# Kernel tuning notes

Hardware: AMD Instinct MI355X
Metric: run time of the kernel (lower is better)

## Reference

```python
import jax, jax.numpy as jnp
import numpy as np

PI = np.pi


def _apply_1q(state, gate, wire, n):
    # state: [B, 2**n] complex64; gate: [2,2] (shared) or [B,2,2] (per-sample)
    # PennyLane convention: wire 0 is the most-significant bit of the state index.
    B = state.shape[0]
    left, right = 2 ** wire, 2 ** (n - wire - 1)
    s = state.reshape(B, left, 2, right)
    if gate.ndim == 2:
        s = jnp.einsum('kl,balr->bakr', gate, s)
    else:
        s = jnp.einsum('bkl,balr->bakr', gate, s)
    return s.reshape(B, -1)


def _apply_cz(state, wire, n):
    # CZ on (wire, wire+1): flip sign of |..11..> amplitudes
    B = state.shape[0]
    left, right = 2 ** wire, 2 ** (n - wire - 2)
    s = state.reshape(B, left, 2, 2, right)
    s = s.at[:, :, 1, 1, :].multiply(-1.0)
    return s.reshape(B, -1)


def _ry_batched(theta):
    # theta: [B] -> [B,2,2] complex RY(theta)
    h = 0.5 * theta
    c, s = jnp.cos(h), jnp.sin(h)
    g = jnp.stack([jnp.stack([c, -s], -1), jnp.stack([s, c], -1)], -2)
    return g.astype(jnp.complex64)


def _rot(phi, theta, omega):
    # Rot = RZ(omega) @ RY(theta) @ RZ(phi)
    c, s = jnp.cos(0.5 * theta), jnp.sin(0.5 * theta)
    e_mm = jnp.exp(-0.5j * (phi + omega))
    e_pm = jnp.exp(0.5j * (phi - omega))
    e_mp = jnp.exp(-0.5j * (phi - omega))
    e_pp = jnp.exp(0.5j * (phi + omega))
    g = jnp.stack([jnp.stack([e_mm * c, -e_pm * s]), jnp.stack([e_mp * s, e_pp * c])])
    return g.astype(jnp.complex64)


def _simulate(enc, weights):
    # enc: [B, n_qubits] in [-1,1]; weights: [n_layers, n_qubits, 3]
    n_layers, n, _ = weights.shape
    B = enc.shape[0]
    state = jnp.zeros((B, 2 ** n), jnp.complex64).at[:, 0].set(1.0)
    ry = [_ry_batched(enc[:, i] * PI) for i in range(n)]
    for l in range(n_layers):
        for i in range(n):
            state = _apply_1q(state, ry[i], i, n)
        for i in range(n):
            state = _apply_1q(state, _rot(weights[l, i, 0], weights[l, i, 1], weights[l, i, 2]), i, n)
        for i in range(n - 1):
            state = _apply_cz(state, i, n)
    for i in range(n):
        state = _apply_1q(state, ry[i], i, n)
    probs = state.real ** 2 + state.imag ** 2  # [B, 2**n]
    # <Z_i> = sum_k probs[k] * (-1)^bit_i(k), wire 0 = MSB
    bits = (jnp.arange(2 ** n)[None, :] >> (n - 1 - jnp.arange(n))[:, None]) & 1
    signs = (1 - 2 * bits).astype(probs.dtype)  # [n, 2**n]
    return probs @ signs.T  # [B, n]


def setup_inputs() -> dict:
    B, D, NQ, NL, NA = 32768, 16, 8, 4, 4
    key = jax.random.key(0)
    ks = jax.random.split(key, 6)

    def lin(k, o, i):
        b = 1.0 / np.sqrt(i)
        k1, k2 = jax.random.split(k)
        return (jax.random.uniform(k1, (o, i), jnp.float32, -b, b),
                jax.random.uniform(k2, (o,), jnp.float32, -b, b))

    enc_w1, enc_b1 = lin(ks[1], 8, D)
    enc_w2, enc_b2 = lin(ks[2], NQ, 8)
    dec_w1, dec_b1 = lin(ks[3], 8, NQ)
    dec_w2, dec_b2 = lin(ks[4], NA, 8)
    q_weights = jax.random.uniform(ks[5], (NL, NQ, 3), jnp.float32, 0.0, 2.0 * PI)
    x = jax.random.normal(ks[0], (B, D), jnp.float32)
    return {"x": x, "enc_w1": enc_w1, "enc_b1": enc_b1, "enc_w2": enc_w2, "enc_b2": enc_b2,
            "q_weights": q_weights, "dec_w1": dec_w1, "dec_b1": dec_b1, "dec_w2": dec_w2, "dec_b2": dec_b2}


def reference(x, enc_w1, enc_b1, enc_w2, enc_b2, q_weights, dec_w1, dec_b1, dec_w2, dec_b2):
    h = jax.nn.relu(x @ enc_w1.T + enc_b1)
    enc = jnp.tanh(h @ enc_w2.T + enc_b2)          # [B, n_qubits]
    q = _simulate(enc, q_weights)                  # [B, n_qubits] PauliZ expvals
    h2 = jax.nn.relu(q @ dec_w1.T + dec_b1)
    return h2 @ dec_w2.T + dec_b2                  # [B, n_actions]
```

## Files before the change

kernel.cpp:

```cpp
#include <hip/hip_runtime.h>
#include <math.h>


#define PI_F 3.14159265358979323846f

typedef float v2f __attribute__((ext_vector_type(2)));

struct C2 { float re, im; };
__device__ __forceinline__ C2 cmul(C2 a, C2 b) {
    C2 r;
    r.re = fmaf(a.re, b.re, -a.im * b.im);
    r.im = fmaf(a.re, b.im,  a.im * b.re);
    return r;
}

__device__ __forceinline__ v2f pk_mul(v2f a, v2f b) {
    v2f d; asm("v_pk_mul_f32 %0, %1, %2" : "=v"(d) : "v"(a), "v"(b)); return d;
}
__device__ __forceinline__ v2f pk_mul_neg(v2f a, v2f b) {
    v2f d; asm("v_pk_mul_f32 %0, %1, %2 neg_lo:[1,0] neg_hi:[1,0]"
               : "=v"(d) : "v"(a), "v"(b)); return d;
}
__device__ __forceinline__ v2f pk_fma(v2f a, v2f b, v2f c) {
    v2f d; asm("v_pk_fma_f32 %0, %1, %2, %3" : "=v"(d) : "v"(a), "v"(b), "v"(c)); return d;
}
__device__ __forceinline__ v2f pk_fma_nn(v2f a, v2f b, v2f c) {
    v2f d; asm("v_pk_fma_f32 %0, %1, %2, %3 neg_lo:[1,0,0] neg_hi:[1,0,0]"
               : "=v"(d) : "v"(a), "v"(b), "v"(c)); return d;
}
__device__ __forceinline__ v2f pk_fma_swl(v2f a, v2f b, v2f c) {
    v2f d; asm("v_pk_fma_f32 %0, %1, %2, %3 op_sel:[0,1,0] op_sel_hi:[1,0,1] neg_lo:[1,0,0]"
               : "=v"(d) : "v"(a), "v"(b), "v"(c)); return d;
}
__device__ __forceinline__ v2f pk_fma_swh(v2f a, v2f b, v2f c) {
    v2f d; asm("v_pk_fma_f32 %0, %1, %2, %3 op_sel:[0,1,0] op_sel_hi:[1,0,1] neg_hi:[1,0,0]"
               : "=v"(d) : "v"(a), "v"(b), "v"(c)); return d;
}

template<int CTRL>
__device__ __forceinline__ float dppf(float x) {
    int xi = __float_as_int(x);
    int r = __builtin_amdgcn_update_dpp(xi, xi, CTRL, 0xF, 0xF, false);
    return __int_as_float(r);
}
template<int M>
__device__ __forceinline__ float lxor(float x) {
    if constexpr (M == 1)      return dppf<0xB1>(x);
    else if constexpr (M == 2) return dppf<0x4E>(x);
    else if constexpr (M == 4) return __int_as_float(
        __builtin_amdgcn_ds_swizzle(__float_as_int(x), 0x101F));
    else                       return dppf<0x128>(x);
}

__device__ __forceinline__ void build_G(const float* __restrict__ c_lds, int g,
                                        float cc, float ss,
                                        v2f& arr, v2f& aii, v2f& brr, v2f& bii) {
    const float4 c0 = *(const float4*)(c_lds + 4 * g);
    float ar = fmaf(c0.x, cc, -c0.z * ss);
    float ai = fmaf(c0.y, cc,  c0.w * ss);
    float br = fmaf(c0.z, cc,  c0.x * ss);
    float bi = fmaf(c0.w, cc, -c0.y * ss);
    arr = (v2f){ar, ar}; aii = (v2f){ai, ai};
    brr = (v2f){br, br}; bii = (v2f){bi, bi};
}

template<int ST>
__device__ __forceinline__ void su2_inlane(v2f arr, v2f aii, v2f brr, v2f bii,
                                           v2f z[16]) {
#pragma unroll
    for (int t = 0; t < 16; t++) {
        if ((t & ST) == 0) {
            const int u = t + ST;
            v2f x = z[t], y = z[u];
            v2f nx = pk_mul(arr, x);
            nx = pk_fma_swl(aii, x, nx);
            nx = pk_fma_nn (brr, y, nx);
            nx = pk_fma_swl(bii, y, nx);
            v2f ny = pk_mul(brr, x);
            ny = pk_fma_swl(bii, x, ny);
            ny = pk_fma   (arr, y, ny);
            ny = pk_fma_swh(aii, y, ny);
            z[t] = nx; z[u] = ny;
        }
    }
}

template<int ST>
__device__ __forceinline__ void ry_inlane(v2f cc, v2f ss, v2f z[16]) {
#pragma unroll
    for (int t = 0; t < 16; t++) {
        if ((t & ST) == 0) {
            const int u = t + ST;
            v2f x = z[t], y = z[u];
            z[t] = pk_fma_nn(ss, y, pk_mul(cc, x));
            z[u] = pk_fma   (cc, y, pk_mul(ss, x));
        }
    }
}

__device__ __constant__ const bool CZNEG[16] =
    { false,false,false,true,  false,false,true,false,
      false,false,false,true,  true, true, false,true };

__global__ __launch_bounds__(128) void qdqn_kernel(
    const float* __restrict__ x,
    const float* __restrict__ ew1, const float* __restrict__ eb1,
    const float* __restrict__ ew2, const float* __restrict__ eb2,
    const float* __restrict__ qw,
    const float* __restrict__ dw1, const float* __restrict__ db1,
    const float* __restrict__ dw2, const float* __restrict__ db2,
    float* __restrict__ out, int B, int NL) {
    __shared__ __align__(16) float c_lds[32 * 4];
    __shared__ __align__(16) v2f tbuf[2 * 4 * 288];

    const int tid = threadIdx.x;
    const int n_gates = NL * 8;

    if (tid < n_gates) {
        const int g = tid;
        float phi = qw[3 * g + 0], th = qw[3 * g + 1], om = qw[3 * g + 2];
        float c = __cosf(0.5f * th), s = __sinf(0.5f * th);
        float A = 0.5f * (phi + om), Bb = 0.5f * (phi - om);
        float* o = c_lds + 4 * g;
        o[0] =  __cosf(A) * c;  o[1] = -__sinf(A) * c;
        o[2] =  __cosf(Bb) * s; o[3] = -__sinf(Bb) * s;
    }
    __syncthreads();

    const int wave = tid >> 6;
    const int lane = tid & 63;
    const int grp = lane >> 4;
    const int L = lane & 15;
    int s = blockIdx.x * 8 + wave * 4 + grp;
    if (s >= B) s = B - 1;
    v2f* tb = &tbuf[(wave * 4 + grp) * 288];

    float xv[16];
    const float4* xp = (const float4*)(x + s * 16);
#pragma unroll
    for (int i = 0; i < 4; i++) {
        float4 v = xp[i];
        xv[4*i] = v.x; xv[4*i+1] = v.y; xv[4*i+2] = v.z; xv[4*i+3] = v.w;
    }
    float hbuf[8];
#pragma unroll
    for (int j = 0; j < 8; j++) {
        float a = eb1[j];
#pragma unroll
        for (int i = 0; i < 16; i++) a = fmaf(ew1[j * 16 + i], xv[i], a);
        hbuf[j] = fmaxf(a, 0.0f);
    }
    float cq[8], sq[8];
#pragma unroll
    for (int q = 0; q < 8; q++) {
        float a = eb2[q];
#pragma unroll
        for (int j = 0; j < 8; j++) a = fmaf(ew2[q * 8 + j], hbuf[j], a);
        float e = 1.0f - __fdividef(2.0f, __expf(2.0f * a) + 1.0f);
        float ang = e * (0.5f * PI_F);
        cq[q] = __cosf(ang);
        sq[q] = __sinf(ang);
    }

    const int L0 = L & 1, L1b = (L >> 1) & 1, L2b = (L >> 2) & 1, L3b = (L >> 3) & 1;
    const int cnt = (L3b & L2b) + (L2b & L1b) + (L1b & L0);
    const float mL = (cnt & 1) ? -1.0f : 1.0f;
    const float mH = L0 ? -mL : mL;
    const float mO = L3b ? -mL : mL;
    const v2f mL2 = (v2f){mL, mL}, mH2 = (v2f){mH, mH}, mO2 = (v2f){mO, mO};

    v2f z[16];
    {
        C2 P; P.re = 1.0f; P.im = 0.0f;
        C2 F[4][2];
#pragma unroll
        for (int q = 0; q < 8; q++) {
            const float4 c0 = *(const float4*)(c_lds + 4 * q);
            float ar = fmaf(c0.x, cq[q], -c0.z * sq[q]);
            float ai = fmaf(c0.y, cq[q],  c0.w * sq[q]);
            float br = fmaf(c0.z, cq[q],  c0.x * sq[q]);
            float bi = fmaf(c0.w, cq[q], -c0.y * sq[q]);
            if (q < 4) {
                const bool hi = (L >> (3 - q)) & 1;
                C2 f; f.re = hi ? br : ar; f.im = hi ? bi : ai;
                P = cmul(P, f);
            } else {
                F[q-4][0].re = ar; F[q-4][0].im = ai;
                F[q-4][1].re = br; F[q-4][1].im = bi;
            }
        }
        C2 A0 = cmul(P, F[0][0]), A1 = cmul(P, F[0][1]);
        C2 Bv[4];
        Bv[0] = cmul(A0, F[1][0]); Bv[1] = cmul(A0, F[1][1]);
        Bv[2] = cmul(A1, F[1][0]); Bv[3] = cmul(A1, F[1][1]);
        C2 Cv[8];
#pragma unroll
        for (int i = 0; i < 8; i++) Cv[i] = cmul(Bv[i >> 1], F[2][i & 1]);
#pragma unroll
        for (int t = 0; t < 16; t++) {
            C2 v = cmul(Cv[t >> 1], F[3][t & 1]);
            float m = (t < 8) ? mL : mH;
            m = CZNEG[t] ? -m : m;
            z[t].x = v.re * m;
            z[t].y = v.im * m;
        }
    }

    auto transpose = [&]() {
        float4* wrow = (float4*)(tb + L * 18);
#pragma unroll
        for (int k = 0; k < 8; k++)
            wrow[k] = make_float4(z[2*k].x, z[2*k].y, z[2*k+1].x, z[2*k+1].y);
        __builtin_amdgcn_wave_barrier();
#pragma unroll
        for (int j = 0; j < 16; j++) z[j] = tb[j * 18 + L];
        __builtin_amdgcn_wave_barrier();
    };

    auto cz_A = [&]() {
#pragma unroll
        for (int t = 0; t < 16; t++) {
            v2f m = (t < 8) ? mL2 : mH2;
            z[t] = CZNEG[t] ? pk_mul_neg(m, z[t]) : pk_mul(m, z[t]);
        }
    };
    auto cz_B = [&]() {
#pragma unroll
        for (int j = 0; j < 16; j++) {
            v2f m = (j & 1) ? mO2 : mL2;
            z[j] = CZNEG[j] ? pk_mul_neg(m, z[j]) : pk_mul(m, z[j]);
        }
    };

    v2f arr, aii, brr, bii;
    bool inB = false;
    for (int l = 1; l < NL; l++) {
        const int g0 = l * 8;
        if (!inB) {
            build_G(c_lds, g0+4, cq[4], sq[4], arr, aii, brr, bii); su2_inlane<8>(arr, aii, brr, bii, z);
            build_G(c_lds, g0+5, cq[5], sq[5], arr, aii, brr, bii); su2_inlane<4>(arr, aii, brr, bii, z);
            build_G(c_lds, g0+6, cq[6], sq[6], arr, aii, brr, bii); su2_inlane<2>(arr, aii, brr, bii, z);
            build_G(c_lds, g0+7, cq[7], sq[7], arr, aii, brr, bii); su2_inlane<1>(arr, aii, brr, bii, z);
            transpose();
            build_G(c_lds, g0+0, cq[0], sq[0], arr, aii, brr, bii); su2_inlane<8>(arr, aii, brr, bii, z);
            build_G(c_lds, g0+1, cq[1], sq[1], arr, aii, brr, bii); su2_inlane<4>(arr, aii, brr, bii, z);
            build_G(c_lds, g0+2, cq[2], sq[2], arr, aii, brr, bii); su2_inlane<2>(arr, aii, brr, bii, z);
            build_G(c_lds, g0+3, cq[3], sq[3], arr, aii, brr, bii); su2_inlane<1>(arr, aii, brr, bii, z);
            cz_B();
            inB = true;
        } else {
            build_G(c_lds, g0+0, cq[0], sq[0], arr, aii, brr, bii); su2_inlane<8>(arr, aii, brr, bii, z);
            build_G(c_lds, g0+1, cq[1], sq[1], arr, aii, brr, bii); su2_inlane<4>(arr, aii, brr, bii, z);
            build_G(c_lds, g0+2, cq[2], sq[2], arr, aii, brr, bii); su2_inlane<2>(arr, aii, brr, bii, z);
            build_G(c_lds, g0+3, cq[3], sq[3], arr, aii, brr, bii); su2_inlane<1>(arr, aii, brr, bii, z);
            transpose();
            build_G(c_lds, g0+4, cq[4], sq[4], arr, aii, brr, bii); su2_inlane<8>(arr, aii, brr, bii, z);
            build_G(c_lds, g0+5, cq[5], sq[5], arr, aii, brr, bii); su2_inlane<4>(arr, aii, brr, bii, z);
            build_G(c_lds, g0+6, cq[6], sq[6], arr, aii, brr, bii); su2_inlane<2>(arr, aii, brr, bii, z);
            build_G(c_lds, g0+7, cq[7], sq[7], arr, aii, brr, bii); su2_inlane<1>(arr, aii, brr, bii, z);
            cz_A();
            inB = false;
        }
    }

    {
        v2f cc, ss;
        if (inB) {
            cc=(v2f){cq[0],cq[0]}; ss=(v2f){sq[0],sq[0]}; ry_inlane<8>(cc, ss, z);
            cc=(v2f){cq[1],cq[1]}; ss=(v2f){sq[1],sq[1]}; ry_inlane<4>(cc, ss, z);
            cc=(v2f){cq[2],cq[2]}; ss=(v2f){sq[2],sq[2]}; ry_inlane<2>(cc, ss, z);
            cc=(v2f){cq[3],cq[3]}; ss=(v2f){sq[3],sq[3]}; ry_inlane<1>(cc, ss, z);
            transpose();
            cc=(v2f){cq[4],cq[4]}; ss=(v2f){sq[4],sq[4]}; ry_inlane<8>(cc, ss, z);
            cc=(v2f){cq[5],cq[5]}; ss=(v2f){sq[5],sq[5]}; ry_inlane<4>(cc, ss, z);
            cc=(v2f){cq[6],cq[6]}; ss=(v2f){sq[6],sq[6]}; ry_inlane<2>(cc, ss, z);
            cc=(v2f){cq[7],cq[7]}; ss=(v2f){sq[7],sq[7]}; ry_inlane<1>(cc, ss, z);
        } else {
            cc=(v2f){cq[4],cq[4]}; ss=(v2f){sq[4],sq[4]}; ry_inlane<8>(cc, ss, z);
            cc=(v2f){cq[5],cq[5]}; ss=(v2f){sq[5],sq[5]}; ry_inlane<4>(cc, ss, z);
            cc=(v2f){cq[6],cq[6]}; ss=(v2f){sq[6],sq[6]}; ry_inlane<2>(cc, ss, z);
            cc=(v2f){cq[7],cq[7]}; ss=(v2f){sq[7],sq[7]}; ry_inlane<1>(cc, ss, z);
            transpose();
            cc=(v2f){cq[0],cq[0]}; ss=(v2f){sq[0],sq[0]}; ry_inlane<8>(cc, ss, z);
            cc=(v2f){cq[1],cq[1]}; ss=(v2f){sq[1],sq[1]}; ry_inlane<4>(cc, ss, z);
            cc=(v2f){cq[2],cq[2]}; ss=(v2f){sq[2],sq[2]}; ry_inlane<2>(cc, ss, z);
            cc=(v2f){cq[3],cq[3]}; ss=(v2f){sq[3],sq[3]}; ry_inlane<1>(cc, ss, z);
            transpose();
        }
    }

    float p[16];
#pragma unroll
    for (int t = 0; t < 16; t++) p[t] = fmaf(z[t].x, z[t].x, z[t].y * z[t].y);

    float e0 = p[0]+p[1],  e1 = p[2]+p[3],  e2 = p[4]+p[5],  e3 = p[6]+p[7];
    float e4 = p[8]+p[9],  e5 = p[10]+p[11], e6 = p[12]+p[13], e7 = p[14]+p[15];
    float q0 = e0+e1, q1 = e2+e3, q2 = e4+e5, q3 = e6+e7;
    float h0 = q0+q1, h1 = q2+q3;
    float sumP = h0 + h1;

    float zv[8];
#pragma unroll
    for (int w = 0; w < 4; w++)
        zv[w] = ((L >> (3 - w)) & 1) ? -sumP : sumP;
    zv[4] = h0 - h1;
    zv[5] = (q0 - q1) + (q2 - q3);
    zv[6] = (e0 - e1) + (e2 - e3) + (e4 - e5) + (e6 - e7);
    zv[7] = (p[0]-p[1]) + (p[2]-p[3]) + (p[4]-p[5]) + (p[6]-p[7])
          + (p[8]-p[9]) + (p[10]-p[11]) + (p[12]-p[13]) + (p[14]-p[15]);

#pragma unroll
    for (int w = 0; w < 8; w++) zv[w] += lxor<1>(zv[w]);
#pragma unroll
    for (int w = 0; w < 8; w++) zv[w] += lxor<2>(zv[w]);
#pragma unroll
    for (int w = 0; w < 8; w++) zv[w] += lxor<4>(zv[w]);
#pragma unroll
    for (int w = 0; w < 8; w++) zv[w] += lxor<8>(zv[w]);

    float h2[8];
#pragma unroll
    for (int j = 0; j < 8; j++) {
        float a = db1[j];
#pragma unroll
        for (int w = 0; w < 8; w++) a = fmaf(dw1[j * 8 + w], zv[w], a);
        h2[j] = fmaxf(a, 0.0f);
    }
    if (L < 4) {
        float a = db2[L];
#pragma unroll
        for (int j = 0; j < 8; j++) a = fmaf(dw2[L * 8 + j], h2[j], a);
        out[s * 4 + L] = a;
    }
}

extern "C" void kernel_launch(void* const* d_in, const int* in_sizes, int n_in,
                              void* d_out, int out_size, void* d_ws, size_t ws_size,
                              hipStream_t stream) {
    const float* x   = (const float*)d_in[0];
    const float* ew1 = (const float*)d_in[1];
    const float* eb1 = (const float*)d_in[2];
    const float* ew2 = (const float*)d_in[3];
    const float* eb2 = (const float*)d_in[4];
    const float* qw  = (const float*)d_in[5];
    const float* dw1 = (const float*)d_in[6];
    const float* db1 = (const float*)d_in[7];
    const float* dw2 = (const float*)d_in[8];
    const float* db2 = (const float*)d_in[9];
    float* out = (float*)d_out;

    int B = in_sizes[0] / 16;
    int n_gates = in_sizes[5] / 3;
    int NL = n_gates / 8;

    int blocks = (B + 7) / 8;
    qdqn_kernel<<<blocks, 128, 0, stream>>>(x, ew1, eb1, ew2, eb2, qw,
                                            dw1, db1, dw2, db2, out, B, NL);
}
```

Baseline: 121.6 us.

## Replace LDS transposes with cross-lane DPP/swizzle gate application on high qubits

The LDS-based transpose, which moved the state between two layouts, is removed. The four high qubits are now applied directly across lanes using DPP/ds_swizzle xor exchanges, with sign masks folded into the gate coefficients. This drops the shared-memory staging buffer and the layout-parity tracking, and the block size grows from 128 to 256 threads with 16 samples per block. In exchange, every element of each high-qubit gate now needs cross-lane moves plus more packed FMAs than the in-lane butterfly.

```diff
diff --git a/kernel.cpp b/kernel.cpp
--- a/kernel.cpp
+++ b/kernel.cpp
@@ -12,6 +12,9 @@
     r.re = fmaf(a.re, b.re, -a.im * b.im);
     r.im = fmaf(a.re, b.im,  a.im * b.re);
     return r;
+}
+__device__ __forceinline__ float fxor(float x, int m) {
+    return __int_as_float(__float_as_int(x) ^ m);
 }
 
 __device__ __forceinline__ v2f pk_mul(v2f a, v2f b) {
@@ -52,16 +55,30 @@
     else                       return dppf<0x128>(x);
 }
 
-__device__ __forceinline__ void build_G(const float* __restrict__ c_lds, int g,
+__device__ __forceinline__ void load_G2(const float* __restrict__ c_lds, int g,
                                         float cc, float ss,
-                                        v2f& arr, v2f& aii, v2f& brr, v2f& bii) {
+                                        float& ar, float& ai, float& br, float& bi) {
     const float4 c0 = *(const float4*)(c_lds + 4 * g);
-    float ar = fmaf(c0.x, cc, -c0.z * ss);
-    float ai = fmaf(c0.y, cc,  c0.w * ss);
-    float br = fmaf(c0.z, cc,  c0.x * ss);
-    float bi = fmaf(c0.w, cc, -c0.y * ss);
-    arr = (v2f){ar, ar}; aii = (v2f){ai, ai};
-    brr = (v2f){br, br}; bii = (v2f){bi, bi};
+    ar = fmaf(c0.x, cc, -c0.z * ss);
+    ai = fmaf(c0.y, cc,  c0.w * ss);
+    br = fmaf(c0.z, cc,  c0.x * ss);
+    bi = fmaf(c0.w, cc, -c0.y * ss);
+}
+
+template<int M>
+__device__ __forceinline__ void su2_cross(v2f cSr, v2f cSi, v2f cOr, v2f cOi,
+                                          v2f z[16]) {
+#pragma unroll
+    for (int t = 0; t < 16; t++) {
+        v2f p;
+        p.x = lxor<M>(z[t].x);
+        p.y = lxor<M>(z[t].y);
+        v2f n = pk_mul(cSr, z[t]);
+        n = pk_fma_swl(cSi, z[t], n);
+        n = pk_fma   (cOr, p, n);
+        n = pk_fma_swl(cOi, p, n);
+        z[t] = n;
+    }
 }
 
 template<int ST>
@@ -85,6 +102,16 @@
     }
 }
 
+template<int M>
+__device__ __forceinline__ void ry_cross(v2f cc, v2f cO, v2f z[16]) {
+#pragma unroll
+    for (int t = 0; t < 16; t++) {
+        v2f p;
+        p.x = lxor<M>(z[t].x);
+        p.y = lxor<M>(z[t].y);
+        z[t] = pk_fma(cO, p, pk_mul(cc, z[t]));
+    }
+}
 template<int ST>
 __device__ __forceinline__ void ry_inlane(v2f cc, v2f ss, v2f z[16]) {
 #pragma unroll
@@ -102,7 +129,7 @@
     { false,false,false,true,  false,false,true,false,
       false,false,false,true,  true, true, false,true };
 
-__global__ __launch_bounds__(128) void qdqn_kernel(
+__global__ __launch_bounds__(256) void qdqn_kernel(
     const float* __restrict__ x,
     const float* __restrict__ ew1, const float* __restrict__ eb1,
     const float* __restrict__ ew2, const float* __restrict__ eb2,
@@ -111,7 +138,6 @@
     const float* __restrict__ dw2, const float* __restrict__ db2,
     float* __restrict__ out, int B, int NL) {
     __shared__ __align__(16) float c_lds[32 * 4];
-    __shared__ __align__(16) v2f tbuf[2 * 4 * 288];
 
     const int tid = threadIdx.x;
     const int n_gates = NL * 8;
@@ -127,13 +153,10 @@
     }
     __syncthreads();
 
-    const int wave = tid >> 6;
     const int lane = tid & 63;
-    const int grp = lane >> 4;
     const int L = lane & 15;
-    int s = blockIdx.x * 8 + wave * 4 + grp;
+    int s = blockIdx.x * 16 + (tid >> 4);
     if (s >= B) s = B - 1;
-    v2f* tb = &tbuf[(wave * 4 + grp) * 288];
 
     float xv[16];
     const float4* xp = (const float4*)(x + s * 16);
@@ -162,12 +185,19 @@
         sq[q] = __sinf(ang);
     }
 
+    int hiM[4], loM[4];
+#pragma unroll
+    for (int q = 0; q < 4; q++) {
+        int hi = (L >> (3 - q)) & 1;
+        hiM[q] = hi << 31;
+        loM[q] = hiM[q] ^ 0x80000000;
+    }
+
     const int L0 = L & 1, L1b = (L >> 1) & 1, L2b = (L >> 2) & 1, L3b = (L >> 3) & 1;
     const int cnt = (L3b & L2b) + (L2b & L1b) + (L1b & L0);
     const float mL = (cnt & 1) ? -1.0f : 1.0f;
     const float mH = L0 ? -mL : mL;
-    const float mO = L3b ? -mL : mL;
-    const v2f mL2 = (v2f){mL, mL}, mH2 = (v2f){mH, mH}, mO2 = (v2f){mO, mO};
+    const v2f mL2 = (v2f){mL, mL}, mH2 = (v2f){mH, mH};
 
     v2f z[16];
     {
@@ -175,11 +205,8 @@
         C2 F[4][2];
 #pragma unroll
         for (int q = 0; q < 8; q++) {
-            const float4 c0 = *(const float4*)(c_lds + 4 * q);
-            float ar = fmaf(c0.x, cq[q], -c0.z * sq[q]);
-            float ai = fmaf(c0.y, cq[q],  c0.w * sq[q]);
-            float br = fmaf(c0.z, cq[q],  c0.x * sq[q]);
-            float bi = fmaf(c0.w, cq[q], -c0.y * sq[q]);
+            float ar, ai, br, bi;
+            load_G2(c_lds, q, cq[q], sq[q], ar, ai, br, bi);
             if (q < 4) {
                 const bool hi = (L >> (3 - q)) & 1;
                 C2 f; f.re = hi ? br : ar; f.im = hi ? bi : ai;
@@ -206,87 +233,50 @@
         }
     }
 
-    auto transpose = [&]() {
-        float4* wrow = (float4*)(tb + L * 18);
-#pragma unroll
-        for (int k = 0; k < 8; k++)
-            wrow[k] = make_float4(z[2*k].x, z[2*k].y, z[2*k+1].x, z[2*k+1].y);
-        __builtin_amdgcn_wave_barrier();
-#pragma unroll
-        for (int j = 0; j < 16; j++) z[j] = tb[j * 18 + L];
-        __builtin_amdgcn_wave_barrier();
-    };
-
-    auto cz_A = [&]() {
+    for (int l = 1; l < NL; l++) {
+        const int g0 = l * 8;
+        float ar, ai, br, bi;
+        load_G2(c_lds, g0+0, cq[0], sq[0], ar, ai, br, bi);
+        su2_cross<8>((v2f){ar,ar}, (v2f){fxor(ai,hiM[0]),fxor(ai,hiM[0])},
+                     (v2f){fxor(br,loM[0]),fxor(br,loM[0])}, (v2f){bi,bi}, z);
+        load_G2(c_lds, g0+1, cq[1], sq[1], ar, ai, br, bi);
+        su2_cross<4>((v2f){ar,ar}, (v2f){fxor(ai,hiM[1]),fxor(ai,hiM[1])},
+                     (v2f){fxor(br,loM[1]),fxor(br,loM[1])}, (v2f){bi,bi}, z);
+        load_G2(c_lds, g0+2, cq[2], sq[2], ar, ai, br, bi);
+        su2_cross<2>((v2f){ar,ar}, (v2f){fxor(ai,hiM[2]),fxor(ai,hiM[2])},
+                     (v2f){fxor(br,loM[2]),fxor(br,loM[2])}, (v2f){bi,bi}, z);
+        load_G2(c_lds, g0+3, cq[3], sq[3], ar, ai, br, bi);
+        su2_cross<1>((v2f){ar,ar}, (v2f){fxor(ai,hiM[3]),fxor(ai,hiM[3])},
+                     (v2f){fxor(br,loM[3]),fxor(br,loM[3])}, (v2f){bi,bi}, z);
+        load_G2(c_lds, g0+4, cq[4], sq[4], ar, ai, br, bi);
+        su2_inlane<8>((v2f){ar,ar}, (v2f){ai,ai}, (v2f){br,br}, (v2f){bi,bi}, z);
+        load_G2(c_lds, g0+5, cq[5], sq[5], ar, ai, br, bi);
+        su2_inlane<4>((v2f){ar,ar}, (v2f){ai,ai}, (v2f){br,br}, (v2f){bi,bi}, z);
+        load_G2(c_lds, g0+6, cq[6], sq[6], ar, ai, br, bi);
+        su2_inlane<2>((v2f){ar,ar}, (v2f){ai,ai}, (v2f){br,br}, (v2f){bi,bi}, z);
+        load_G2(c_lds, g0+7, cq[7], sq[7], ar, ai, br, bi);
+        su2_inlane<1>((v2f){ar,ar}, (v2f){ai,ai}, (v2f){br,br}, (v2f){bi,bi}, z);
 #pragma unroll
         for (int t = 0; t < 16; t++) {
             v2f m = (t < 8) ? mL2 : mH2;
             z[t] = CZNEG[t] ? pk_mul_neg(m, z[t]) : pk_mul(m, z[t]);
         }
-    };
-    auto cz_B = [&]() {
-#pragma unroll
-        for (int j = 0; j < 16; j++) {
-            v2f m = (j & 1) ? mO2 : mL2;
-            z[j] = CZNEG[j] ? pk_mul_neg(m, z[j]) : pk_mul(m, z[j]);
-        }
-    };
-
-    v2f arr, aii, brr, bii;
-    bool inB = false;
-    for (int l = 1; l < NL; l++) {
-        const int g0 = l * 8;
-        if (!inB) {
-            build_G(c_lds, g0+4, cq[4], sq[4], arr, aii, brr, bii); su2_inlane<8>(arr, aii, brr, bii, z);
-            build_G(c_lds, g0+5, cq[5], sq[5], arr, aii, brr, bii); su2_inlane<4>(arr, aii, brr, bii, z);
-            build_G(c_lds, g0+6, cq[6], sq[6], arr, aii, brr, bii); su2_inlane<2>(arr, aii, brr, bii, z);
-            build_G(c_lds, g0+7, cq[7], sq[7], arr, aii, brr, bii); su2_inlane<1>(arr, aii, brr, bii, z);
-            transpose();
-            build_G(c_lds, g0+0, cq[0], sq[0], arr, aii, brr, bii); su2_inlane<8>(arr, aii, brr, bii, z);
-            build_G(c_lds, g0+1, cq[1], sq[1], arr, aii, brr, bii); su2_inlane<4>(arr, aii, brr, bii, z);
-            build_G(c_lds, g0+2, cq[2], sq[2], arr, aii, brr, bii); su2_inlane<2>(arr, aii, brr, bii, z);
-            build_G(c_lds, g0+3, cq[3], sq[3], arr, aii, brr, bii); su2_inlane<1>(arr, aii, brr, bii, z);
-            cz_B();
-            inB = true;
-        } else {
-            build_G(c_lds, g0+0, cq[0], sq[0], arr, aii, brr, bii); su2_inlane<8>(arr, aii, brr, bii, z);
-            build_G(c_lds, g0+1, cq[1], sq[1], arr, aii, brr, bii); su2_inlane<4>(arr, aii, brr, bii, z);
-            build_G(c_lds, g0+2, cq[2], sq[2], arr, aii, brr, bii); su2_inlane<2>(arr, aii, brr, bii, z);
-            build_G(c_lds, g0+3, cq[3], sq[3], arr, aii, brr, bii); su2_inlane<1>(arr, aii, brr, bii, z);
-            transpose();
-            build_G(c_lds, g0+4, cq[4], sq[4], arr, aii, brr, bii); su2_inlane<8>(arr, aii, brr, bii, z);
-            build_G(c_lds, g0+5, cq[5], sq[5], arr, aii, brr, bii); su2_inlane<4>(arr, aii, brr, bii, z);
-            build_G(c_lds, g0+6, cq[6], sq[6], arr, aii, brr, bii); su2_inlane<2>(arr, aii, brr, bii, z);
-            build_G(c_lds, g0+7, cq[7], sq[7], arr, aii, brr, bii); su2_inlane<1>(arr, aii, brr, bii, z);
-            cz_A();
-            inB = false;
-        }
     }
 
     {
-        v2f cc, ss;
-        if (inB) {
-            cc=(v2f){cq[0],cq[0]}; ss=(v2f){sq[0],sq[0]}; ry_inlane<8>(cc, ss, z);
-            cc=(v2f){cq[1],cq[1]}; ss=(v2f){sq[1],sq[1]}; ry_inlane<4>(cc, ss, z);
-            cc=(v2f){cq[2],cq[2]}; ss=(v2f){sq[2],sq[2]}; ry_inlane<2>(cc, ss, z);
-            cc=(v2f){cq[3],cq[3]}; ss=(v2f){sq[3],sq[3]}; ry_inlane<1>(cc, ss, z);
-            transpose();
-            cc=(v2f){cq[4],cq[4]}; ss=(v2f){sq[4],sq[4]}; ry_inlane<8>(cc, ss, z);
-            cc=(v2f){cq[5],cq[5]}; ss=(v2f){sq[5],sq[5]}; ry_inlane<4>(cc, ss, z);
-            cc=(v2f){cq[6],cq[6]}; ss=(v2f){sq[6],sq[6]}; ry_inlane<2>(cc, ss, z);
-            cc=(v2f){cq[7],cq[7]}; ss=(v2f){sq[7],sq[7]}; ry_inlane<1>(cc, ss, z);
-        } else {
-            cc=(v2f){cq[4],cq[4]}; ss=(v2f){sq[4],sq[4]}; ry_inlane<8>(cc, ss, z);
-            cc=(v2f){cq[5],cq[5]}; ss=(v2f){sq[5],sq[5]}; ry_inlane<4>(cc, ss, z);
-            cc=(v2f){cq[6],cq[6]}; ss=(v2f){sq[6],sq[6]}; ry_inlane<2>(cc, ss, z);
-            cc=(v2f){cq[7],cq[7]}; ss=(v2f){sq[7],sq[7]}; ry_inlane<1>(cc, ss, z);
-            transpose();
-            cc=(v2f){cq[0],cq[0]}; ss=(v2f){sq[0],sq[0]}; ry_inlane<8>(cc, ss, z);
-            cc=(v2f){cq[1],cq[1]}; ss=(v2f){sq[1],sq[1]}; ry_inlane<4>(cc, ss, z);
-            cc=(v2f){cq[2],cq[2]}; ss=(v2f){sq[2],sq[2]}; ry_inlane<2>(cc, ss, z);
-            cc=(v2f){cq[3],cq[3]}; ss=(v2f){sq[3],sq[3]}; ry_inlane<1>(cc, ss, z);
-            transpose();
-        }
+        v2f cc, cO, ss;
+        cc=(v2f){cq[0],cq[0]}; cO=(v2f){fxor(sq[0],loM[0]),fxor(sq[0],loM[0])};
+        ry_cross<8>(cc, cO, z);
+        cc=(v2f){cq[1],cq[1]}; cO=(v2f){fxor(sq[1],loM[1]),fxor(sq[1],loM[1])};
+        ry_cross<4>(cc, cO, z);
+        cc=(v2f){cq[2],cq[2]}; cO=(v2f){fxor(sq[2],loM[2]),fxor(sq[2],loM[2])};
+        ry_cross<2>(cc, cO, z);
+        cc=(v2f){cq[3],cq[3]}; cO=(v2f){fxor(sq[3],loM[3]),fxor(sq[3],loM[3])};
+        ry_cross<1>(cc, cO, z);
+        cc=(v2f){cq[4],cq[4]}; ss=(v2f){sq[4],sq[4]}; ry_inlane<8>(cc, ss, z);
+        cc=(v2f){cq[5],cq[5]}; ss=(v2f){sq[5],sq[5]}; ry_inlane<4>(cc, ss, z);
+        cc=(v2f){cq[6],cq[6]}; ss=(v2f){sq[6],sq[6]}; ry_inlane<2>(cc, ss, z);
+        cc=(v2f){cq[7],cq[7]}; ss=(v2f){sq[7],sq[7]}; ry_inlane<1>(cc, ss, z);
     }
 
     float p[16];
@@ -353,7 +343,7 @@
     int n_gates = in_sizes[5] / 3;
     int NL = n_gates / 8;
 
-    int blocks = (B + 7) / 8;
-    qdqn_kernel<<<blocks, 128, 0, stream>>>(x, ew1, eb1, ew2, eb2, qw,
+    int blocks = (B + 15) / 16;
+    qdqn_kernel<<<blocks, 256, 0, stream>>>(x, ew1, eb1, ew2, eb2, qw,
                                             dw1, db1, dw2, db2, out, B, NL);
 }
```

New measurement: 124.1 us. +2.0%, slower.
